# Kernel optimization log

Hardware: AMD Instinct MI355X
Metric: run time of the kernel (lower is better)

## Reference

```python
import jax, jax.numpy as jnp
import numpy as np

C_M, C_Z, C = 256, 128, 32
LN_EPS = 1e-5


def setup_inputs() -> dict:
    key = jax.random.key(0)
    ks = jax.random.split(key, 9)
    S, R = 128, 384  # N_seq, N_res
    m = jax.random.normal(ks[0], (S, R, C_M), dtype=jnp.float32)
    ln_g = jnp.ones((C_M,), jnp.float32)
    ln_b = jnp.zeros((C_M,), jnp.float32)
    w1 = jax.random.normal(ks[1], (C_M, C), jnp.float32) / np.sqrt(C_M)
    b1 = jnp.zeros((C,), jnp.float32)
    w2 = jax.random.normal(ks[2], (C_M, C), jnp.float32) / np.sqrt(C_M)
    b2 = jnp.zeros((C,), jnp.float32)
    w_out = jax.random.normal(ks[3], (C * C, C_Z), jnp.float32) / np.sqrt(C * C)
    b_out = jnp.zeros((C_Z,), jnp.float32)
    return {"m": m, "ln_g": ln_g, "ln_b": ln_b, "w1": w1, "b1": b1,
            "w2": w2, "b2": b2, "w_out": w_out, "b_out": b_out}


def reference(m, ln_g, ln_b, w1, b1, w2, b2, w_out, b_out):
    S, R, _ = m.shape
    # LayerNorm over c_m
    mu = jnp.mean(m, axis=-1, keepdims=True)
    var = jnp.var(m, axis=-1, keepdims=True)
    mn = (m - mu) * jax.lax.rsqrt(var + LN_EPS) * ln_g + ln_b
    a = mn @ w1 + b1  # (S, R, c)
    b = mn @ w2 + b2  # (S, R, c)
    # outer product summed over N_seq: out[i,j,x,y] = sum_s a[s,i,x] b[s,j,y]
    o = jnp.einsum('six,sjy->ijxy', a, b)  # (R, R, c, c)
    o = o.reshape(R, R, C * C) @ w_out + b_out  # (R, R, c_z)
    return o / S
```

## Files before the change

### kernel.cpp

```cpp
#include <hip/hip_runtime.h>
#include <hip/hip_bf16.h>

#define R_RES 384
#define S_SEQ 128
#define CM 256
#define CC 32
#define CZ 128

typedef __attribute__((ext_vector_type(8))) short bf16x8;
typedef __attribute__((ext_vector_type(4))) float f32x4;
typedef __attribute__((ext_vector_type(16))) float f32x16;
typedef __attribute__((ext_vector_type(4))) int i32x4;

__device__ __forceinline__ short tobf16(float f) {
    union { __hip_bfloat16 h; short s; } u;
    u.h = __float2bfloat16(f);
    return u.s;
}

__device__ __forceinline__ void lgkm_barrier() {
    asm volatile("s_waitcnt lgkmcnt(0)" ::: "memory");
    __builtin_amdgcn_s_barrier();
    __builtin_amdgcn_sched_barrier(0);
}

__global__ void k_transpose_wout(const float* __restrict__ w_out, short* __restrict__ wbTf) {
    __shared__ float t[64][65];
    int k0 = blockIdx.x * 64;
    int z0 = blockIdx.y * 64;
    int tid = threadIdx.x;
    int c = tid & 63, rg = tid >> 6;
#pragma unroll
    for (int rr = 0; rr < 16; ++rr) {
        int kk = rg * 16 + rr;
        t[kk][c] = w_out[(size_t)(k0 + kk) * CZ + z0 + c];
    }
    __syncthreads();
#pragma unroll
    for (int l = 0; l < 2; ++l) {
        int id = l * 256 + tid;
        int f = id >> 6;
        int ksl = f >> 1, fzl = f & 1;
        int ln = id & 63;
        int zl = fzl * 32 + (ln & 31);
        int kl = ksl * 16 + (ln >> 5) * 8;
        bf16x8 pk;
#pragma unroll
        for (int j = 0; j < 8; ++j) pk[j] = tobf16(t[kl + j][zl]);
        size_t fz = blockIdx.y * 2 + fzl;
        size_t ks16 = blockIdx.x * 4 + ksl;
        *(bf16x8*)(wbTf + ((fz * 64 + ks16) * 64 + ln) * 8) = pk;
    }
}

__global__ void k_pack_w12(const float* __restrict__ w1, const float* __restrict__ w2,
                           short* __restrict__ wcT) {
    int idx = blockIdx.x * 256 + threadIdx.x;
    int k = idx >> 6, n = idx & 63;
    float v = (n < 32) ? w1[k * CC + n] : w2[k * CC + (n - 32)];
    wcT[n * CM + k] = tobf16(v);
}

__global__ __launch_bounds__(256) void k_ln_proj(
    const float* __restrict__ M, const float* __restrict__ ln_g, const float* __restrict__ ln_b,
    const float* __restrict__ b1, const float* __restrict__ b2,
    const short* __restrict__ wcT, short* __restrict__ aTf, short* __restrict__ bTf) {
    __shared__ short mnb[64 * 256];
    __shared__ short ab_s[2][32 * 72];
    int r = blockIdx.x >> 1;
    int s0 = (blockIdx.x & 1) * 64;
    int tid = threadIdx.x, lane = tid & 63, w = tid >> 6;
    int g = lane >> 4, r16 = lane & 15;
    float4 gv = *(const float4*)(ln_g + lane * 4);
    float4 bv = *(const float4*)(ln_b + lane * 4);
    for (int it = 0; it < 16; ++it) {
        int sl = it * 4 + w;
        float4 v = *(const float4*)(M + ((size_t)(s0 + sl) * R_RES + r) * CM + lane * 4);
        float sum = v.x + v.y + v.z + v.w;
        float sq = v.x * v.x + v.y * v.y + v.z * v.z + v.w * v.w;
#pragma unroll
        for (int off = 32; off; off >>= 1) {
            sum += __shfl_xor(sum, off);
            sq  += __shfl_xor(sq, off);
        }
        float mu = sum * (1.0f / 256.0f);
        float var = sq * (1.0f / 256.0f) - mu * mu;
        float rstd = rsqrtf(var + 1e-5f);
        short4 mnp;
        mnp.x = tobf16((v.x - mu) * rstd * gv.x + bv.x);
        mnp.y = tobf16((v.y - mu) * rstd * gv.y + bv.y);
        mnp.z = tobf16((v.z - mu) * rstd * gv.z + bv.z);
        mnp.w = tobf16((v.w - mu) * rstd * gv.w + bv.w);
        int byte = sl * 512 + lane * 8;
        byte ^= ((sl & 7) << 4);
        *(short4*)((char*)mnb + byte) = mnp;
    }
    __syncthreads();
    f32x4 acc[4] = {{0,0,0,0},{0,0,0,0},{0,0,0,0},{0,0,0,0}};
    int srow = w * 16 + r16;
#pragma unroll
    for (int ks = 0; ks < 8; ++ks) {
        int byte = srow * 512 + ks * 64 + g * 16;
        byte ^= ((srow & 7) << 4);
        bf16x8 af = *(const bf16x8*)((const char*)mnb + byte);
#pragma unroll
        for (int nt = 0; nt < 4; ++nt) {
            bf16x8 bf = *(const bf16x8*)(wcT + (nt * 16 + r16) * CM + ks * 32 + g * 8);
            acc[nt] = __builtin_amdgcn_mfma_f32_16x16x32_bf16(af, bf, acc[nt], 0, 0, 0);
        }
    }
#pragma unroll
    for (int nt = 0; nt < 4; ++nt) {
        int n = nt * 16 + r16;
        int x = n & 31, sel = n >> 5;
        float bias = sel ? b2[x] : b1[x];
#pragma unroll
        for (int rr = 0; rr < 4; ++rr) {
            int sl = w * 16 + g * 4 + rr;
            ab_s[sel][x * 72 + sl] = tobf16(acc[nt][rr] + bias);
        }
    }
    __syncthreads();
    int piece = tid >> 6;
    int fl = piece >> 1, kl = piece & 1;
    int ln = tid & 63;
    int x = fl * 16 + (ln & 15);
    int s_loc = kl * 32 + (ln >> 4) * 8;
    i32x4 va = *(const i32x4*)((const char*)ab_s[0] + (x * 72 + s_loc) * 2);
    i32x4 vb = *(const i32x4*)((const char*)ab_s[1] + (x * 72 + s_loc) * 2);
    size_t off = ((((size_t)r * 2 + fl) * 4 + (s0 >> 5) + kl) * 64 + ln) * 16;
    *(i32x4*)((char*)aTf + off) = va;
    *(i32x4*)((char*)bTf + off) = vb;
}

__global__ __launch_bounds__(512, 4) void k_opm(
    const short* __restrict__ aTf, const short* __restrict__ bTf,
    const short* __restrict__ wbTf, const float* __restrict__ b_out,
    float* __restrict__ out) {
    __shared__ __align__(16) char smem[65536];
    int tid = threadIdx.x, lane = tid & 63, w = tid >> 6;
    int g = lane >> 4, r16 = lane & 15;
    int l32 = lane & 31, h = lane >> 5;
    int wm = w;
    int bj = blockIdx.x, bi = blockIdx.y;

    const char* gB = (const char*)bTf + (size_t)bj * 32768;
#pragma unroll
    for (int it = 0; it < 4; ++it) {
        int q = it * 8192 + tid * 16;
        __builtin_amdgcn_global_load_lds(
            (const __attribute__((address_space(1))) void*)(gB + q),
            (__attribute__((address_space(3))) void*)(smem + q), 16, 0, 0);
    }
    const char* gA = (const char*)aTf + (size_t)bi * 65536;
    bf16x8 afc0 = *(const bf16x8*)(gA + (((wm * 2 + 0) * 4 + 0) * 64 + lane) * 16);
    bf16x8 afc1 = *(const bf16x8*)(gA + (((wm * 2 + 1) * 4 + 0) * 64 + lane) * 16);
    __syncthreads();

    f32x4 acc[2][8] = {};
#pragma unroll
    for (int ks = 0; ks < 4; ++ks) {
        int ksn = (ks + 1) & 3;
        bf16x8 bf[8];
#pragma unroll
        for (int ni = 0; ni < 4; ++ni)
            bf[ni] = *(const bf16x8*)(smem + ((ni * 4 + ks) * 64 + lane) * 16);
        bf16x8 afn0 = *(const bf16x8*)(gA + (((wm * 2 + 0) * 4 + ksn) * 64 + lane) * 16);
        bf16x8 afn1 = *(const bf16x8*)(gA + (((wm * 2 + 1) * 4 + ksn) * 64 + lane) * 16);
        __builtin_amdgcn_s_setprio(1);
#pragma unroll
        for (int ni = 0; ni < 4; ++ni) {
            acc[0][ni] = __builtin_amdgcn_mfma_f32_16x16x32_bf16(bf[ni], afc0, acc[0][ni], 0, 0, 0);
            acc[1][ni] = __builtin_amdgcn_mfma_f32_16x16x32_bf16(bf[ni], afc1, acc[1][ni], 0, 0, 0);
        }
        __builtin_amdgcn_s_setprio(0);
#pragma unroll
        for (int ni = 4; ni < 8; ++ni)
            bf[ni] = *(const bf16x8*)(smem + ((ni * 4 + ks) * 64 + lane) * 16);
        __builtin_amdgcn_s_setprio(1);
#pragma unroll
        for (int ni = 4; ni < 8; ++ni) {
            acc[0][ni] = __builtin_amdgcn_mfma_f32_16x16x32_bf16(bf[ni], afc0, acc[0][ni], 0, 0, 0);
            acc[1][ni] = __builtin_amdgcn_mfma_f32_16x16x32_bf16(bf[ni], afc1, acc[1][ni], 0, 0, 0);
        }
        __builtin_amdgcn_s_setprio(0);
        afc0 = afn0;
        afc1 = afn1;
    }
    lgkm_barrier();

#pragma unroll
    for (int mi = 0; mi < 2; ++mi)
#pragma unroll
        for (int ni = 0; ni < 8; ++ni) {
            int x = mi * 16 + r16;
            int nb = ni * 16 + g * 4;
            int j = nb >> 5, y0 = nb & 31;
            int p = wm * 4 + j;
            int byte = (p * 2048 + x * 64 + y0 * 2) ^ (((p & 7) ^ (x & 7)) << 4);
            short4 pk;
            pk.x = tobf16(acc[mi][ni][0]);
            pk.y = tobf16(acc[mi][ni][1]);
            pk.z = tobf16(acc[mi][ni][2]);
            pk.w = tobf16(acc[mi][ni][3]);
            *(short4*)(smem + byte) = pk;
        }

    int kh = w & 1, zq = w >> 1;
    const short* wbase = wbTf + (size_t)((zq * 64 + kh * 32) * 64) * 8;
    bf16x8 wpf[4];
#pragma unroll
    for (int u = 0; u < 4; ++u)
        wpf[u] = *(const bf16x8*)(wbase + (u * 64 + lane) * 8);
    lgkm_barrier();

    f32x16 c2a = {0,0,0,0,0,0,0,0,0,0,0,0,0,0,0,0};
    f32x16 c2b = {0,0,0,0,0,0,0,0,0,0,0,0,0,0,0,0};
#pragma unroll
    for (int kq = 0; kq < 8; ++kq) {
        bf16x8 w0 = wpf[0], w1 = wpf[1], w2 = wpf[2], w3 = wpf[3];
        if (kq < 7) {
#pragma unroll
            for (int u = 0; u < 4; ++u)
                wpf[u] = *(const bf16x8*)(wbase + ((kq * 4 + 4 + u) * 64 + lane) * 8);
        }
        bf16x8 a2f[4];
#pragma unroll
        for (int u = 0; u < 4; ++u) {
            int ks = kq * 4 + u;
            int x = (kh * 32 + ks) >> 1;
            int byte = (l32 * 2048 + kh * 1024 + ks * 32 + h * 16)
                       ^ ((((l32 & 7) ^ (x & 7))) << 4);
            a2f[u] = *(const bf16x8*)(smem + byte);
        }
        __builtin_amdgcn_s_setprio(1);
        c2a = __builtin_amdgcn_mfma_f32_32x32x16_bf16(a2f[0], w0, c2a, 0, 0, 0);
        c2b = __builtin_amdgcn_mfma_f32_32x32x16_bf16(a2f[1], w1, c2b, 0, 0, 0);
        c2a = __builtin_amdgcn_mfma_f32_32x32x16_bf16(a2f[2], w2, c2a, 0, 0, 0);
        c2b = __builtin_amdgcn_mfma_f32_32x32x16_bf16(a2f[3], w3, c2b, 0, 0, 0);
        __builtin_amdgcn_s_setprio(0);
    }
    f32x16 c2 = c2a + c2b;
    lgkm_barrier();

#pragma unroll
    for (int q = 0; q < 4; ++q) {
        f32x4 v;
        v[0] = c2[q * 4 + 0]; v[1] = c2[q * 4 + 1];
        v[2] = c2[q * 4 + 2]; v[3] = c2[q * 4 + 3];
        int byte = ((zq * 2 + kh) * 4096 + l32 * 128 + q * 32 + h * 16) ^ ((l32 & 7) << 4);
        *(f32x4*)(smem + byte) = v;
    }
    lgkm_barrier();

    int z = tid & 127, zq2 = z >> 5, zp = z & 31;
    int pr0 = tid >> 7;
    float bo = b_out[z];
#pragma unroll
    for (int stp = 0; stp < 2; ++stp) {
        int prq = pr0 + stp * 4;
        int base = zq2 * 8192 + zp * 128 + prq * 16;
        int sw = (zp & 7) << 4;
        f32x4 v0 = *(const f32x4*)(smem + (base ^ sw));
        f32x4 v1 = *(const f32x4*)(smem + ((base + 4096) ^ sw));
#pragma unroll
        for (int rr = 0; rr < 4; ++rr) {
            int p = prq * 4 + rr;
            int ig = bi * 8 + (p >> 2);
            int jg = bj * 4 + (p & 3);
            out[((size_t)ig * R_RES + jg) * CZ + z] = (v0[rr] + v1[rr] + bo) * (1.0f / 128.0f);
        }
    }
}

extern "C" void kernel_launch(void* const* d_in, const int* in_sizes, int n_in,
                              void* d_out, int out_size, void* d_ws, size_t ws_size,
                              hipStream_t stream) {
    const float* M     = (const float*)d_in[0];
    const float* ln_g  = (const float*)d_in[1];
    const float* ln_b  = (const float*)d_in[2];
    const float* w1    = (const float*)d_in[3];
    const float* b1    = (const float*)d_in[4];
    const float* w2    = (const float*)d_in[5];
    const float* b2    = (const float*)d_in[6];
    const float* w_out = (const float*)d_in[7];
    const float* b_out = (const float*)d_in[8];
    float* out = (float*)d_out;

    short* aTf  = (short*)d_ws;
    short* bTf  = aTf + 12288 * 128;
    short* wbTf = bTf + 12288 * 128;
    short* wcT  = wbTf + 128 * 1024;

    k_transpose_wout<<<dim3(16, 2), 256, 0, stream>>>(w_out, wbTf);
    k_pack_w12<<<64, 256, 0, stream>>>(w1, w2, wcT);
    k_ln_proj<<<768, 256, 0, stream>>>(M, ln_g, ln_b, b1, b2, wcT, aTf, bTf);
    k_opm<<<dim3(96, 48), 512, 0, stream>>>(aTf, bTf, wbTf, b_out, out);
}
```

Baseline: 128.1 us.

## Switch outer-product stage to 32x32x16 MFMA with new fragment layout and vectorized stores

Re-packs the a/b projections into a 16-wide k-slice fragment layout suited to 32x32x16 MFMA, and rewrites the first outer-product GEMM to use four 32x32 accumulators per wave instead of sixteen 16x16 tiles. The LDS swizzle for the intermediate bf16 tile gains an extra XOR term. The final reduction is transposed so each thread writes eight contiguous z outputs as two float4 stores. The aim is fewer MFMA issues and LDS reads per FLOP and wider global stores. The cost is a layout change that has to stay consistent across kernels, plus some dead code left in the projection kernel.

```diff
diff --git a/kernel.cpp b/kernel.cpp
--- a/kernel.cpp
+++ b/kernel.cpp
@@ -48,8 +48,8 @@
 #pragma unroll
         for (int j = 0; j < 8; ++j) pk[j] = tobf16(t[kl + j][zl]);
         size_t fz = blockIdx.y * 2 + fzl;
-        size_t ks16 = blockIdx.x * 4 + ksl;
-        *(bf16x8*)(wbTf + ((fz * 64 + ks16) * 64 + ln) * 8) = pk;
+        size_t k16 = blockIdx.x * 4 + ksl;
+        *(bf16x8*)(wbTf + ((fz * 64 + k16) * 64 + ln) * 8) = pk;
     }
 }
 
@@ -121,16 +121,38 @@
         }
     }
     __syncthreads();
-    int piece = tid >> 6;
-    int fl = piece >> 1, kl = piece & 1;
-    int ln = tid & 63;
-    int x = fl * 16 + (ln & 15);
-    int s_loc = kl * 32 + (ln >> 4) * 8;
-    i32x4 va = *(const i32x4*)((const char*)ab_s[0] + (x * 72 + s_loc) * 2);
-    i32x4 vb = *(const i32x4*)((const char*)ab_s[1] + (x * 72 + s_loc) * 2);
-    size_t off = ((((size_t)r * 2 + fl) * 4 + (s0 >> 5) + kl) * 64 + ln) * 16;
-    *(i32x4*)((char*)aTf + off) = va;
-    *(i32x4*)((char*)bTf + off) = vb;
+#pragma unroll
+    for (int f = 0; f < 2; ++f) {
+        int ks16 = (tid >> 6) * 2 + f;
+        int ln = tid & 63;
+        int xr = ln & 31;
+        int sx = ks16 * 16 + (ln >> 5) * 8;
+        if ((ks16 >> 2) == 0) {
+            int gks = (s0 >> 4) + ks16;
+            int sl = sx;
+            i32x4 va = *(const i32x4*)((const char*)ab_s[0] + (xr * 72 + sl) * 2);
+            i32x4 vb = *(const i32x4*)((const char*)ab_s[1] + (xr * 72 + sl) * 2);
+            size_t off = (((size_t)r * 8 + gks) * 64 + ln) * 16;
+            *(i32x4*)((char*)aTf + off) = va;
+            *(i32x4*)((char*)bTf + off) = vb;
+        } else {
+            int gks = (s0 >> 4) + (ks16 & 3);
+            int sl = (ks16 & 3) * 16 + (ln >> 5) * 8 + 8;
+            (void)gks; (void)sl;
+        }
+    }
+    {
+        int lf = tid >> 6;
+        int ln = tid & 63;
+        int xr = ln & 31;
+        int sl = lf * 16 + (ln >> 5) * 8;
+        int gks = (s0 >> 4) + lf;
+        i32x4 va = *(const i32x4*)((const char*)ab_s[0] + (xr * 72 + sl) * 2);
+        i32x4 vb = *(const i32x4*)((const char*)ab_s[1] + (xr * 72 + sl) * 2);
+        size_t off = (((size_t)r * 8 + gks) * 64 + ln) * 16;
+        *(i32x4*)((char*)aTf + off) = va;
+        *(i32x4*)((char*)bTf + off) = vb;
+    }
 }
 
 __global__ __launch_bounds__(512, 4) void k_opm(
@@ -139,9 +161,7 @@
     float* __restrict__ out) {
     __shared__ __align__(16) char smem[65536];
     int tid = threadIdx.x, lane = tid & 63, w = tid >> 6;
-    int g = lane >> 4, r16 = lane & 15;
     int l32 = lane & 31, h = lane >> 5;
-    int wm = w;
     int bj = blockIdx.x, bi = blockIdx.y;
 
     const char* gB = (const char*)bTf + (size_t)bj * 32768;
@@ -153,123 +173,129 @@
             (__attribute__((address_space(3))) void*)(smem + q), 16, 0, 0);
     }
     const char* gA = (const char*)aTf + (size_t)bi * 65536;
-    bf16x8 afc0 = *(const bf16x8*)(gA + (((wm * 2 + 0) * 4 + 0) * 64 + lane) * 16);
-    bf16x8 afc1 = *(const bf16x8*)(gA + (((wm * 2 + 1) * 4 + 0) * 64 + lane) * 16);
+    bf16x8 afc = *(const bf16x8*)(gA + (w * 8 + 0) * 1024 + lane * 16);
+    asm volatile("s_waitcnt vmcnt(0)" ::: "memory");
     __syncthreads();
 
-    f32x4 acc[2][8] = {};
-#pragma unroll
-    for (int ks = 0; ks < 4; ++ks) {
-        int ksn = (ks + 1) & 3;
-        bf16x8 bf[8];
+    f32x16 acc[4] = {};
+#pragma unroll
+    for (int ks = 0; ks < 8; ++ks) {
+        bf16x8 bf[4];
 #pragma unroll
         for (int ni = 0; ni < 4; ++ni)
-            bf[ni] = *(const bf16x8*)(smem + ((ni * 4 + ks) * 64 + lane) * 16);
-        bf16x8 afn0 = *(const bf16x8*)(gA + (((wm * 2 + 0) * 4 + ksn) * 64 + lane) * 16);
-        bf16x8 afn1 = *(const bf16x8*)(gA + (((wm * 2 + 1) * 4 + ksn) * 64 + lane) * 16);
+            bf[ni] = *(const bf16x8*)(smem + ((ni * 8 + ks) * 1024 + lane * 16));
+        bf16x8 afn = afc;
+        if (ks < 7) afn = *(const bf16x8*)(gA + (w * 8 + ks + 1) * 1024 + lane * 16);
         __builtin_amdgcn_s_setprio(1);
 #pragma unroll
-        for (int ni = 0; ni < 4; ++ni) {
-            acc[0][ni] = __builtin_amdgcn_mfma_f32_16x16x32_bf16(bf[ni], afc0, acc[0][ni], 0, 0, 0);
-            acc[1][ni] = __builtin_amdgcn_mfma_f32_16x16x32_bf16(bf[ni], afc1, acc[1][ni], 0, 0, 0);
-        }
+        for (int ni = 0; ni < 4; ++ni)
+            acc[ni] = __builtin_amdgcn_mfma_f32_32x32x16_bf16(bf[ni], afc, acc[ni], 0, 0, 0);
         __builtin_amdgcn_s_setprio(0);
-#pragma unroll
-        for (int ni = 4; ni < 8; ++ni)
-            bf[ni] = *(const bf16x8*)(smem + ((ni * 4 + ks) * 64 + lane) * 16);
-        __builtin_amdgcn_s_setprio(1);
-#pragma unroll
-        for (int ni = 4; ni < 8; ++ni) {
-            acc[0][ni] = __builtin_amdgcn_mfma_f32_16x16x32_bf16(bf[ni], afc0, acc[0][ni], 0, 0, 0);
-            acc[1][ni] = __builtin_amdgcn_mfma_f32_16x16x32_bf16(bf[ni], afc1, acc[1][ni], 0, 0, 0);
-        }
-        __builtin_amdgcn_s_setprio(0);
-        afc0 = afn0;
-        afc1 = afn1;
+        afc = afn;
     }
     lgkm_barrier();
 
 #pragma unroll
-    for (int mi = 0; mi < 2; ++mi)
-#pragma unroll
-        for (int ni = 0; ni < 8; ++ni) {
-            int x = mi * 16 + r16;
-            int nb = ni * 16 + g * 4;
-            int j = nb >> 5, y0 = nb & 31;
-            int p = wm * 4 + j;
-            int byte = (p * 2048 + x * 64 + y0 * 2) ^ (((p & 7) ^ (x & 7)) << 4);
+    for (int ni = 0; ni < 4; ++ni) {
+        int p = w * 4 + ni;
+        int x = l32;
+        int key = ((p & 7) ^ (x & 7) ^ ((x >> 3) & 3)) << 4;
+#pragma unroll
+        for (int q = 0; q < 4; ++q) {
+            int y0 = 4 * h + 8 * q;
+            int byte = (p * 2048 + x * 64 + y0 * 2) ^ key;
             short4 pk;
-            pk.x = tobf16(acc[mi][ni][0]);
-            pk.y = tobf16(acc[mi][ni][1]);
-            pk.z = tobf16(acc[mi][ni][2]);
-            pk.w = tobf16(acc[mi][ni][3]);
+            pk.x = tobf16(acc[ni][q * 4 + 0]);
+            pk.y = tobf16(acc[ni][q * 4 + 1]);
+            pk.z = tobf16(acc[ni][q * 4 + 2]);
+            pk.w = tobf16(acc[ni][q * 4 + 3]);
             *(short4*)(smem + byte) = pk;
         }
+    }
 
     int kh = w & 1, zq = w >> 1;
     const short* wbase = wbTf + (size_t)((zq * 64 + kh * 32) * 64) * 8;
-    bf16x8 wpf[4];
+    bf16x8 wcur[4], wnxt[4];
 #pragma unroll
     for (int u = 0; u < 4; ++u)
-        wpf[u] = *(const bf16x8*)(wbase + (u * 64 + lane) * 8);
+        wcur[u] = *(const bf16x8*)(wbase + ((u) * 64 + lane) * 8);
     lgkm_barrier();
 
-    f32x16 c2a = {0,0,0,0,0,0,0,0,0,0,0,0,0,0,0,0};
-    f32x16 c2b = {0,0,0,0,0,0,0,0,0,0,0,0,0,0,0,0};
+    f32x16 c2a = {}, c2b = {};
 #pragma unroll
     for (int kq = 0; kq < 8; ++kq) {
-        bf16x8 w0 = wpf[0], w1 = wpf[1], w2 = wpf[2], w3 = wpf[3];
         if (kq < 7) {
 #pragma unroll
             for (int u = 0; u < 4; ++u)
-                wpf[u] = *(const bf16x8*)(wbase + ((kq * 4 + 4 + u) * 64 + lane) * 8);
+                wnxt[u] = *(const bf16x8*)(wbase + ((kq * 4 + 4 + u) * 64 + lane) * 8);
         }
         bf16x8 a2f[4];
 #pragma unroll
         for (int u = 0; u < 4; ++u) {
-            int ks = kq * 4 + u;
-            int x = (kh * 32 + ks) >> 1;
-            int byte = (l32 * 2048 + kh * 1024 + ks * 32 + h * 16)
-                       ^ ((((l32 & 7) ^ (x & 7))) << 4);
+            int ks16 = kq * 4 + u;
+            int x = kh * 16 + (ks16 >> 1);
+            int y0 = (ks16 & 1) * 16 + h * 8;
+            int key = ((l32 & 7) ^ (x & 7) ^ ((x >> 3) & 3)) << 4;
+            int byte = (l32 * 2048 + x * 64 + y0 * 2) ^ key;
             a2f[u] = *(const bf16x8*)(smem + byte);
         }
         __builtin_amdgcn_s_setprio(1);
-        c2a = __builtin_amdgcn_mfma_f32_32x32x16_bf16(a2f[0], w0, c2a, 0, 0, 0);
-        c2b = __builtin_amdgcn_mfma_f32_32x32x16_bf16(a2f[1], w1, c2b, 0, 0, 0);
-        c2a = __builtin_amdgcn_mfma_f32_32x32x16_bf16(a2f[2], w2, c2a, 0, 0, 0);
-        c2b = __builtin_amdgcn_mfma_f32_32x32x16_bf16(a2f[3], w3, c2b, 0, 0, 0);
+        c2a = __builtin_amdgcn_mfma_f32_32x32x16_bf16(a2f[0], wcur[0], c2a, 0, 0, 0);
+        c2b = __builtin_amdgcn_mfma_f32_32x32x16_bf16(a2f[1], wcur[1], c2b, 0, 0, 0);
+        c2a = __builtin_amdgcn_mfma_f32_32x32x16_bf16(a2f[2], wcur[2], c2a, 0, 0, 0);
+        c2b = __builtin_amdgcn_mfma_f32_32x32x16_bf16(a2f[3], wcur[3], c2b, 0, 0, 0);
         __builtin_amdgcn_s_setprio(0);
+        if (kq < 7) {
+#pragma unroll
+            for (int u = 0; u < 4; ++u) wcur[u] = wnxt[u];
+        }
     }
     f32x16 c2 = c2a + c2b;
     lgkm_barrier();
 
-#pragma unroll
-    for (int q = 0; q < 4; ++q) {
-        f32x4 v;
-        v[0] = c2[q * 4 + 0]; v[1] = c2[q * 4 + 1];
-        v[2] = c2[q * 4 + 2]; v[3] = c2[q * 4 + 3];
-        int byte = ((zq * 2 + kh) * 4096 + l32 * 128 + q * 32 + h * 16) ^ ((l32 & 7) << 4);
-        *(f32x4*)(smem + byte) = v;
+    {
+        int z = zq * 32 + l32;
+        int zkey = (z & 7) << 4;
+#pragma unroll
+        for (int q = 0; q < 4; ++q) {
+            int p0 = 4 * h + 8 * q;
+            int byte = (kh * 16384 + z * 128 + p0 * 4) ^ zkey;
+            f32x4 v;
+            v[0] = c2[q * 4 + 0]; v[1] = c2[q * 4 + 1];
+            v[2] = c2[q * 4 + 2]; v[3] = c2[q * 4 + 3];
+            *(f32x4*)(smem + byte) = v;
+        }
     }
     lgkm_barrier();
 
-    int z = tid & 127, zq2 = z >> 5, zp = z & 31;
-    int pr0 = tid >> 7;
-    float bo = b_out[z];
-#pragma unroll
-    for (int stp = 0; stp < 2; ++stp) {
-        int prq = pr0 + stp * 4;
-        int base = zq2 * 8192 + zp * 128 + prq * 16;
-        int sw = (zp & 7) << 4;
-        f32x4 v0 = *(const f32x4*)(smem + (base ^ sw));
-        f32x4 v1 = *(const f32x4*)(smem + ((base + 4096) ^ sw));
-#pragma unroll
-        for (int rr = 0; rr < 4; ++rr) {
-            int p = prq * 4 + rr;
-            int ig = bi * 8 + (p >> 2);
-            int jg = bj * 4 + (p & 3);
-            out[((size_t)ig * R_RES + jg) * CZ + z] = (v0[rr] + v1[rr] + bo) * (1.0f / 128.0f);
-        }
+    {
+        int p = tid & 31;
+        int z0 = (tid >> 5) * 8;
+        float s[8];
+#pragma unroll
+        for (int i = 0; i < 8; ++i) {
+            int z = z0 + i;
+            int a0 = (z * 128 + p * 4) ^ ((z & 7) << 4);
+            float u0 = *(const float*)(smem + a0);
+            float u1 = *(const float*)(smem + (a0 + 16384));
+            s[i] = u0 + u1;
+        }
+        float4 bo0 = *(const float4*)(b_out + z0);
+        float4 bo1 = *(const float4*)(b_out + z0 + 4);
+        f32x4 r0, r1;
+        r0[0] = (s[0] + bo0.x) * (1.0f / 128.0f);
+        r0[1] = (s[1] + bo0.y) * (1.0f / 128.0f);
+        r0[2] = (s[2] + bo0.z) * (1.0f / 128.0f);
+        r0[3] = (s[3] + bo0.w) * (1.0f / 128.0f);
+        r1[0] = (s[4] + bo1.x) * (1.0f / 128.0f);
+        r1[1] = (s[5] + bo1.y) * (1.0f / 128.0f);
+        r1[2] = (s[6] + bo1.z) * (1.0f / 128.0f);
+        r1[3] = (s[7] + bo1.w) * (1.0f / 128.0f);
+        int ig = bi * 8 + (p >> 2);
+        int jg = bj * 4 + (p & 3);
+        float* po = out + ((size_t)ig * R_RES + jg) * CZ + z0;
+        *(f32x4*)(po) = r0;
+        *(f32x4*)(po + 4) = r1;
     }
 }
 
```

Result: slower. 133.9 us (+4.6%).
